# Performance work log

Measured on AMD Instinct MI355X. Metric: run time of the kernel, lower is better.

## Reference

```python
import jax, jax.numpy as jnp
import numpy as np

HID = 2048
NH = 16
HD = HID // NH
FF = 8192
SEQ = 2048
B = 1
EPS = 1e-05
ROPE_BASE = 10000.0


def _layernorm(x, w, b):
    mu = jnp.mean(x, axis=-1, keepdims=True)
    var = jnp.mean(jnp.square(x - mu), axis=-1, keepdims=True)
    return (x - mu) * jax.lax.rsqrt(var + EPS) * w + b


def _rope(x, offset):
    # x: [B, S, H, D]; rotate-half LLaMA-style rotary embedding
    S, D = x.shape[1], x.shape[3]
    inv_freq = 1.0 / (ROPE_BASE ** (jnp.arange(0, D, 2, dtype=jnp.float32) / D))  # [D/2]
    pos = jnp.arange(S, dtype=jnp.float32) + offset
    ang = pos[:, None] * inv_freq[None, :]                     # [S, D/2]
    cos = jnp.cos(ang)[None, :, None, :]                       # [1,S,1,D/2]
    sin = jnp.sin(ang)[None, :, None, :]
    x1, x2 = x[..., : D // 2], x[..., D // 2 :]
    return jnp.concatenate([x1 * cos - x2 * sin, x2 * cos + x1 * sin], axis=-1)


def setup_inputs() -> dict:
    key = jax.random.key(0)
    ks = jax.random.split(key, 16)
    sd = 0.02
    inp = {
        "hidden_states": jax.random.normal(ks[0], (B, SEQ, HID), dtype=jnp.float32),
        # additive causal mask as fed to multi_head_attention_forward
        "attention_mask": jnp.where(
            jnp.tril(jnp.ones((SEQ, SEQ), dtype=bool)), 0.0, -1e9
        ).astype(jnp.float32),
        "ln1_w": jnp.ones((HID,), jnp.float32),
        "ln1_b": jnp.zeros((HID,), jnp.float32),
        "ln2_w": jnp.ones((HID,), jnp.float32),
        "ln2_b": jnp.zeros((HID,), jnp.float32),
        "wq": jax.random.normal(ks[1], (HID, HID), jnp.float32) * sd,
        "bq": jnp.zeros((HID,), jnp.float32),
        "wk": jax.random.normal(ks[2], (HID, HID), jnp.float32) * sd,
        "bk": jnp.zeros((HID,), jnp.float32),
        "wv": jax.random.normal(ks[3], (HID, HID), jnp.float32) * sd,
        "bv": jnp.zeros((HID,), jnp.float32),
        "wo": jax.random.normal(ks[4], (HID, HID), jnp.float32) * sd,
        "bo": jnp.zeros((HID,), jnp.float32),
        "w_gate": jax.random.normal(ks[5], (FF, HID), jnp.float32) * sd,
        "w_up": jax.random.normal(ks[6], (FF, HID), jnp.float32) * sd,
        "w_down": jax.random.normal(ks[7], (HID, FF), jnp.float32) * sd,
        "total_seq_len": SEQ,
    }
    return inp


def reference(hidden_states, attention_mask, ln1_w, ln1_b, ln2_w, ln2_b,
              wq, bq, wk, bk, wv, bv, wo, bo, w_gate, w_up, w_down,
              total_seq_len):
    Bv, S, _ = hidden_states.shape
    x = _layernorm(hidden_states, ln1_w, ln1_b)
    q = (x @ wq.T + bq).reshape(Bv, S, NH, HD)
    k = (x @ wk.T + bk).reshape(Bv, S, NH, HD)
    v = (x @ wv.T + bv).reshape(Bv, S, NH, HD)
    offset = total_seq_len - S  # 0 for prefill
    q = _rope(q, offset)
    k = _rope(k, offset)
    # cache of max_sequence_length zeros concatenated with k/v then sliced to the
    # last total_seq_len entries == just the current k/v when total_seq_len == S
    scale = 1.0 / np.sqrt(HD)
    scores = jnp.einsum("bshd,bthd->bhst", q, k) * scale + attention_mask[None, None]
    probs = jax.nn.softmax(scores, axis=-1)
    attn = jnp.einsum("bhst,bthd->bshd", probs, v).reshape(Bv, S, HID)
    attn = attn @ wo.T + bo
    h = hidden_states + attn
    y = _layernorm(h, ln2_w, ln2_b)
    ffn = (jax.nn.silu(y @ w_gate.T) * (y @ w_up.T)) @ w_down.T
    return h + ffn
```

## Files before the change

kernel.cpp:

```cpp
#include <hip/hip_runtime.h>

#define HIDN 2048
#define NHEAD 16
#define HDIM 128
#define FFDIM 8192
#define SEQLEN 2048

typedef __attribute__((ext_vector_type(8))) __bf16 bf16x8;
typedef __attribute__((ext_vector_type(4))) float f32x4;
typedef __attribute__((ext_vector_type(4))) unsigned short u16x4;
typedef __attribute__((ext_vector_type(8))) unsigned short u16x8;

__device__ __forceinline__ unsigned short f2bfu(float f) {
    unsigned int u = __float_as_uint(f);
    unsigned int r = u + 0x7fffu + ((u >> 16) & 1u);
    return (unsigned short)(r >> 16);
}
__device__ __forceinline__ float bfu2f(unsigned short u) {
    return __uint_as_float(((unsigned int)u) << 16);
}

__device__ __forceinline__ void gload16(const void* g, void* l) {
    __builtin_amdgcn_global_load_lds(
        (const __attribute__((address_space(1))) unsigned int*)g,
        (__attribute__((address_space(3))) unsigned int*)l,
        16, 0, 0);
}

__global__ __launch_bounds__(256)
void conv_f32_bf16(const float* __restrict__ src, unsigned short* __restrict__ dst) {
    int i = blockIdx.x * 256 + threadIdx.x;
    float4 a = ((const float4*)src)[i * 2];
    float4 b = ((const float4*)src)[i * 2 + 1];
    u16x8 v;
    v[0] = f2bfu(a.x); v[1] = f2bfu(a.y); v[2] = f2bfu(a.z); v[3] = f2bfu(a.w);
    v[4] = f2bfu(b.x); v[5] = f2bfu(b.y); v[6] = f2bfu(b.z); v[7] = f2bfu(b.w);
    *(u16x8*)(dst + (size_t)i * 8) = v;
}

__global__ __launch_bounds__(256)
void conv3_f32_bf16(const float* __restrict__ s0, const float* __restrict__ s1,
                    const float* __restrict__ s2, unsigned short* __restrict__ dst) {
    int i = blockIdx.x * 256 + threadIdx.x;
    int m = i >> 19;
    int li = i & ((1 << 19) - 1);
    const float* s = (m == 0) ? s0 : (m == 1) ? s1 : s2;
    float4 a = ((const float4*)s)[li * 2];
    float4 b = ((const float4*)s)[li * 2 + 1];
    u16x8 v;
    v[0] = f2bfu(a.x); v[1] = f2bfu(a.y); v[2] = f2bfu(a.z); v[3] = f2bfu(a.w);
    v[4] = f2bfu(b.x); v[5] = f2bfu(b.y); v[6] = f2bfu(b.z); v[7] = f2bfu(b.w);
    *(u16x8*)(dst + (size_t)i * 8) = v;
}

__global__ __launch_bounds__(256)
void ln_bf16(const float* __restrict__ x, const float* __restrict__ w,
             const float* __restrict__ b, unsigned short* __restrict__ out) {
    const int row = blockIdx.x;
    const int tid = threadIdx.x;
    const float* xr = x + (size_t)row * HIDN;
    float4 v0 = ((const float4*)xr)[tid];
    float4 v1 = ((const float4*)xr)[tid + 256];
    float s = v0.x + v0.y + v0.z + v0.w + v1.x + v1.y + v1.z + v1.w;
    float q = v0.x*v0.x + v0.y*v0.y + v0.z*v0.z + v0.w*v0.w
            + v1.x*v1.x + v1.y*v1.y + v1.z*v1.z + v1.w*v1.w;
    for (int o = 32; o > 0; o >>= 1) {
        s += __shfl_down(s, o, 64);
        q += __shfl_down(q, o, 64);
    }
    __shared__ float red[8];
    const int wid = tid >> 6;
    if ((tid & 63) == 0) { red[wid] = s; red[4 + wid] = q; }
    __syncthreads();
    float st = red[0] + red[1] + red[2] + red[3];
    float qt = red[4] + red[5] + red[6] + red[7];
    float mu = st * (1.0f / HIDN);
    float var = qt * (1.0f / HIDN) - mu * mu;
    float rs = rsqrtf(var + 1e-5f);
    unsigned short* orow = out + (size_t)row * HIDN;
    int i0 = tid * 4, i1 = (tid + 256) * 4;
    orow[i0 + 0] = f2bfu((v0.x - mu) * rs * w[i0 + 0] + b[i0 + 0]);
    orow[i0 + 1] = f2bfu((v0.y - mu) * rs * w[i0 + 1] + b[i0 + 1]);
    orow[i0 + 2] = f2bfu((v0.z - mu) * rs * w[i0 + 2] + b[i0 + 2]);
    orow[i0 + 3] = f2bfu((v0.w - mu) * rs * w[i0 + 3] + b[i0 + 3]);
    orow[i1 + 0] = f2bfu((v1.x - mu) * rs * w[i1 + 0] + b[i1 + 0]);
    orow[i1 + 1] = f2bfu((v1.y - mu) * rs * w[i1 + 1] + b[i1 + 1]);
    orow[i1 + 2] = f2bfu((v1.z - mu) * rs * w[i1 + 2] + b[i1 + 2]);
    orow[i1 + 3] = f2bfu((v1.w - mu) * rs * w[i1 + 3] + b[i1 + 3]);
}

__global__ __launch_bounds__(256)
void wo_ln(const unsigned short* __restrict__ part, const float* __restrict__ h,
           const float* __restrict__ bo, const float* __restrict__ w,
           const float* __restrict__ b, float* __restrict__ out,
           unsigned short* __restrict__ ybf) {
    const int row = blockIdx.x;
    const int tid = threadIdx.x;
    const int c0 = tid * 4, c1 = (tid + 256) * 4;
    float4 o0 = ((const float4*)(h + (size_t)row * HIDN))[tid];
    float4 o1 = ((const float4*)(h + (size_t)row * HIDN))[tid + 256];
    o0.x += bo[c0]; o0.y += bo[c0 + 1]; o0.z += bo[c0 + 2]; o0.w += bo[c0 + 3];
    o1.x += bo[c1]; o1.y += bo[c1 + 1]; o1.z += bo[c1 + 2]; o1.w += bo[c1 + 3];
#pragma unroll
    for (int sk = 0; sk < 4; ++sk) {
        const unsigned short* pr = part + (size_t)sk * 4194304 + (size_t)row * HIDN;
        u16x4 p0 = *(const u16x4*)(pr + c0);
        u16x4 p1 = *(const u16x4*)(pr + c1);
        o0.x += bfu2f(p0[0]); o0.y += bfu2f(p0[1]); o0.z += bfu2f(p0[2]); o0.w += bfu2f(p0[3]);
        o1.x += bfu2f(p1[0]); o1.y += bfu2f(p1[1]); o1.z += bfu2f(p1[2]); o1.w += bfu2f(p1[3]);
    }
    ((float4*)(out + (size_t)row * HIDN))[tid] = o0;
    ((float4*)(out + (size_t)row * HIDN))[tid + 256] = o1;
    float s = o0.x + o0.y + o0.z + o0.w + o1.x + o1.y + o1.z + o1.w;
    float q = o0.x*o0.x + o0.y*o0.y + o0.z*o0.z + o0.w*o0.w
            + o1.x*o1.x + o1.y*o1.y + o1.z*o1.z + o1.w*o1.w;
    for (int o = 32; o > 0; o >>= 1) {
        s += __shfl_down(s, o, 64);
        q += __shfl_down(q, o, 64);
    }
    __shared__ float red[8];
    const int wid = tid >> 6;
    if ((tid & 63) == 0) { red[wid] = s; red[4 + wid] = q; }
    __syncthreads();
    float st = red[0] + red[1] + red[2] + red[3];
    float qt = red[4] + red[5] + red[6] + red[7];
    float mu = st * (1.0f / HIDN);
    float var = qt * (1.0f / HIDN) - mu * mu;
    float rs = rsqrtf(var + 1e-5f);
    unsigned short* yr = ybf + (size_t)row * HIDN;
    yr[c0 + 0] = f2bfu((o0.x - mu) * rs * w[c0 + 0] + b[c0 + 0]);
    yr[c0 + 1] = f2bfu((o0.y - mu) * rs * w[c0 + 1] + b[c0 + 1]);
    yr[c0 + 2] = f2bfu((o0.z - mu) * rs * w[c0 + 2] + b[c0 + 2]);
    yr[c0 + 3] = f2bfu((o0.w - mu) * rs * w[c0 + 3] + b[c0 + 3]);
    yr[c1 + 0] = f2bfu((o1.x - mu) * rs * w[c1 + 0] + b[c1 + 0]);
    yr[c1 + 1] = f2bfu((o1.y - mu) * rs * w[c1 + 1] + b[c1 + 1]);
    yr[c1 + 2] = f2bfu((o1.z - mu) * rs * w[c1 + 2] + b[c1 + 2]);
    yr[c1 + 3] = f2bfu((o1.w - mu) * rs * w[c1 + 3] + b[c1 + 3]);
}

__global__ __launch_bounds__(256)
void rope_kernel(unsigned short* __restrict__ qk, const int* __restrict__ tsl) {
    int id = blockIdx.x * 256 + threadIdx.x;
    int p  = id & 63;
    int hh = (id >> 6) & 31;
    int s  = id >> 11;
    int off = tsl[0] - SEQLEN;
    float inv = exp2f((float)p * -0.20762050593f);
    float ang = (float)(s + off) * inv;
    float c, sn;
    __sincosf(ang, &sn, &c);
    size_t base = (size_t)s * 4096 + hh * 128 + p;
    float x1 = bfu2f(qk[base]);
    float x2 = bfu2f(qk[base + 64]);
    qk[base]      = f2bfu(x1 * c - x2 * sn);
    qk[base + 64] = f2bfu(x2 * c + x1 * sn);
}

#define BAR __builtin_amdgcn_s_barrier()
#define VM4 asm volatile("s_waitcnt vmcnt(4)" ::: "memory")
#define VM0 asm volatile("s_waitcnt vmcnt(0)" ::: "memory")
#define LGK4 do { asm volatile("s_waitcnt lgkmcnt(4)" ::: "memory"); \
                  __builtin_amdgcn_sched_barrier(0); } while (0)
#define LGK0 do { asm volatile("s_waitcnt lgkmcnt(0)" ::: "memory"); \
                  __builtin_amdgcn_sched_barrier(0); } while (0)

#define STAGE_A(tile, h) { const int k0_ = k_start + (tile) * 64;                      \
  _Pragma("unroll") for (int i_ = 0; i_ < 2; ++i_) {                                   \
    int d_ = (h) * 16384 + i_ * 8192 + tid * 16;                                       \
    int r_ = d_ >> 7;                                                                  \
    int cb_ = (d_ & 127) ^ ((r_ & 7) << 4);                                            \
    gload16((const char*)Ab + ((size_t)(brow + r_) * lda + k0_) * 2 + cb_,             \
            smem + ((tile) & 1) * 65536 + (h) * 16384 + i_ * 8192 + w * 1024); } }

#define STAGE_B(tile, h) { const int k0_ = k_start + (tile) * 64;                      \
  _Pragma("unroll") for (int i_ = 0; i_ < 2; ++i_) {                                   \
    int d_ = (h) * 16384 + i_ * 8192 + tid * 16;                                       \
    int r_ = d_ >> 7;                                                                  \
    int cb_ = (d_ & 127) ^ ((r_ & 7) << 4);                                            \
    gload16((const char*)Bb + ((size_t)(bcol + r_) * ldb + k0_) * 2 + cb_,             \
            smem + ((tile) & 1) * 65536 + 32768 + (h) * 16384 + i_ * 8192 + w * 1024); } }

#define LDB(BO)                                                                        \
  _Pragma("unroll") for (int n_ = 0; n_ < 4; ++n_)                                     \
  _Pragma("unroll") for (int kk_ = 0; kk_ < 2; ++kk_)                                  \
    bF[n_][kk_] = *(const bf16x8*)(smem + (BO) + bbase + n_ * 2048 + colb[kk_]);

#define LDA_SET(BO, MP, SET)                                                           \
  _Pragma("unroll") for (int dm_ = 0; dm_ < 2; ++dm_)                                  \
  _Pragma("unroll") for (int kk_ = 0; kk_ < 2; ++kk_)                                  \
    SET[dm_][kk_] = *(const bf16x8*)(smem + (BO) + abase + ((MP) * 2 + dm_) * 2048 + colb[kk_]);

#define MM_SET(SET, MP)                                                                \
  __builtin_amdgcn_s_setprio(1);                                                       \
  _Pragma("unroll") for (int dm_ = 0; dm_ < 2; ++dm_)                                  \
  _Pragma("unroll") for (int n_ = 0; n_ < 4; ++n_)                                     \
  _Pragma("unroll") for (int kk_ = 0; kk_ < 2; ++kk_)                                  \
    acc[(MP) * 2 + dm_][n_] = __builtin_amdgcn_mfma_f32_16x16x32_bf16(                 \
        SET[dm_][kk_], bF[n_][kk_], acc[(MP) * 2 + dm_][n_], 0, 0, 0);                 \
  __builtin_amdgcn_s_setprio(0);

template<int EPI>
__global__ __launch_bounds__(512, 1)
void gemm256(const unsigned short* __restrict__ Ab, int lda,
             const unsigned short* __restrict__ Bb, int ldb,
             int k_len, int nbx, int ldc,
             const float* __restrict__ bias0, const float* __restrict__ bias1,
             const float* __restrict__ bias2,
             unsigned short* __restrict__ outB, unsigned short* __restrict__ outV) {
    extern __shared__ char smem[];
    const int tid = threadIdx.x;
    const int w = tid >> 6, lane = tid & 63;
    const int lr = lane & 15, lg = lane >> 4;
    const int wrow = (w >> 2) * 128;
    const int wc = w & 3;

    const int cpx = nbx >> 3;
    const int xcd = blockIdx.x & 7;
    const int loc = blockIdx.x >> 3;
    const int bx = xcd * cpx + loc % cpx;
    const int by = loc / cpx;
    const int brow = by * 256, bcol = bx * 256;
    const int k_start = blockIdx.y * k_len;

    const int xorv = (lr & 7) << 4;
    int colb[2];
    colb[0] = (lg * 16) ^ xorv;
    colb[1] = (64 + lg * 16) ^ xorv;
    const int abase = (wrow + lr) * 128;
    const int bbase = 32768 + (wc * 64 + lr) * 128;

    f32x4 acc[8][4];
#pragma unroll
    for (int m = 0; m < 8; ++m)
#pragma unroll
        for (int n = 0; n < 4; ++n) acc[m][n] = (f32x4){0.f, 0.f, 0.f, 0.f};

    bf16x8 bF[4][2], aFa[2][2], aFb[2][2];

    const int NT = k_len >> 6;
    const int NIT = NT >> 1;

    STAGE_A(0, 0); STAGE_A(0, 1); STAGE_B(0, 0); STAGE_B(0, 1);
    STAGE_B(1, 0); STAGE_B(1, 1);
    VM4; BAR;
    LDB(0); LDA_SET(0, 0, aFa);

    for (int it = 0; it < NIT; ++it) {
        const int T = 2 * it;
        const bool s2 = (T + 2) < NT, s3 = (T + 3) < NT;
        STAGE_A(T + 1, 0); LDA_SET(0, 1, aFb); LGK4; MM_SET(aFa, 0);
        STAGE_A(T + 1, 1); LDA_SET(0, 2, aFa); LGK4; MM_SET(aFb, 1);
        BAR;
        if (s2) STAGE_B(T + 2, 0);
        LDA_SET(0, 3, aFb); LGK4; MM_SET(aFa, 2);
        if (s2) STAGE_B(T + 2, 1);
        LGK0; MM_SET(aFb, 3);
        if (s2) { VM4; } else { VM0; }
        BAR;
        LDB(65536); LDA_SET(65536, 0, aFa);
        if (s2) STAGE_A(T + 2, 0);
        LDA_SET(65536, 1, aFb); LGK4; MM_SET(aFa, 0);
        if (s2) STAGE_A(T + 2, 1);
        LDA_SET(65536, 2, aFa); LGK4; MM_SET(aFb, 1);
        BAR;
        if (s3) STAGE_B(T + 3, 0);
        LDA_SET(65536, 3, aFb); LGK4; MM_SET(aFa, 2);
        if (s3) STAGE_B(T + 3, 1);
        LGK0; MM_SET(aFb, 3);
        if (s3) { VM4; } else { VM0; }
        BAR;
        LDB(0); LDA_SET(0, 0, aFa);
    }

    char* sw = smem + w * 16384;
    const bool vblk = (EPI == 0) && (bcol >= 4096);

    if (!vblk) {
#pragma unroll
        for (int n = 0; n < 4; ++n) {
            const int col = bcol + wc * 64 + n * 16 + lr;
            float bv = 0.f;
            if (EPI == 0) bv = (col < 2048) ? bias0[col] : bias1[col - 2048];
#pragma unroll
            for (int m = 0; m < 8; ++m)
#pragma unroll
                for (int j = 0; j < 4; ++j) {
                    const int r = m * 16 + lg * 4 + j;
                    const int cb = ((n * 16 + lr) * 2) ^ ((r & 7) << 4);
                    *(unsigned short*)(sw + r * 128 + cb) = f2bfu(acc[m][n][j] + bv);
                }
        }
        const int rl = lane >> 3, cl = lane & 7;
#pragma unroll
        for (int it2 = 0; it2 < 16; ++it2) {
            const int r = it2 * 8 + rl;
            const int cb = (cl * 16) ^ ((r & 7) << 4);
            u16x8 val = *(const u16x8*)(sw + r * 128 + cb);
            const int gr = brow + wrow + r;
            const int gcol = bcol + wc * 64 + cl * 8;
            if (EPI == 0) {
                *(u16x8*)(outB + (size_t)gr * 4096 + gcol) = val;
            } else if (EPI == 1) {
                *(u16x8*)(outB + (size_t)gr * ldc + gcol) = val;
            } else if (EPI == 3) {
                unsigned short* gp = outB + (size_t)gr * ldc + gcol;
                u16x8 gv = *(const u16x8*)gp;
                u16x8 ov;
#pragma unroll
                for (int e = 0; e < 8; ++e) {
                    float g = bfu2f(gv[e]);
                    float uu = bfu2f(val[e]);
                    ov[e] = f2bfu(g / (1.0f + __expf(-g)) * uu);
                }
                *(u16x8*)gp = ov;
            } else {
                *(u16x8*)(outB + (size_t)blockIdx.y * 4194304 + (size_t)gr * ldc + gcol) = val;
            }
        }
    } else {
#pragma unroll
        for (int n = 0; n < 4; ++n) {
            const int c = n * 16 + lr;
            const float bv = bias2[bcol - 4096 + wc * 64 + c];
            const int cx = (c & 7) << 4;
#pragma unroll
            for (int m = 0; m < 8; ++m) {
                const int r0 = m * 16 + lg * 4;
                u16x4 pk;
#pragma unroll
                for (int j = 0; j < 4; ++j) pk[j] = f2bfu(acc[m][n][j] + bv);
                *(u16x4*)(sw + c * 256 + ((r0 * 2) ^ cx)) = pk;
            }
        }
        const int cg = lane >> 4, rl2 = lane & 15;
#pragma unroll
        for (int it2 = 0; it2 < 16; ++it2) {
            const int c = it2 * 4 + cg;
            const int rb = (rl2 * 16) ^ ((c & 7) << 4);
            u16x8 val = *(const u16x8*)(sw + c * 256 + rb);
            const int d = bcol - 4096 + wc * 64 + c;
            *(u16x8*)(outV + (size_t)d * SEQLEN + brow + wrow + rl2 * 8) = val;
        }
    }
}

__global__ __launch_bounds__(256)
void reduce4_add(const unsigned short* __restrict__ part, float* __restrict__ out) {
    int i = blockIdx.x * 256 + threadIdx.x;
    float4 o = ((const float4*)out)[i];
#pragma unroll
    for (int sk = 0; sk < 4; ++sk) {
        u16x4 p = ((const u16x4*)(part + (size_t)sk * 4194304))[i];
        o.x += bfu2f(p[0]); o.y += bfu2f(p[1]); o.z += bfu2f(p[2]); o.w += bfu2f(p[3]);
    }
    ((float4*)out)[i] = o;
}

#define PST 72
__global__ __launch_bounds__(256)
void attn_kernel(const unsigned short* __restrict__ QK, const unsigned short* __restrict__ VT,
                 unsigned short* __restrict__ O) {
    __shared__ __align__(16) unsigned short Ks[2][64 * 128];
    __shared__ __align__(16) unsigned short Vs[2][128 * 64];
    __shared__ __align__(16) unsigned short Ps[4][16 * PST];
    const int tid = threadIdx.x;
    const int lane = tid & 63;
    const int w = tid >> 6;
    const int lr = lane & 15, lg = lane >> 4;

    const int id = blockIdx.x;
    const int h = ((id & 7) << 1) | ((id >> 3) & 1);
    const int p = id >> 4;

    const unsigned short* Kb = QK + 2048 + h * 128;
    const unsigned short* Vb = VT + (size_t)(h * 128) * SEQLEN;

    int krow[4], kcb[4], vrow[4], vcb[4];
#pragma unroll
    for (int ch = 0; ch < 4; ++ch) {
        int d = ch * 4096 + w * 1024 + lane * 16;
        krow[ch] = d >> 8;
        kcb[ch]  = (d & 255) ^ ((krow[ch] & 7) << 4);
        vrow[ch] = d >> 7;
        vcb[ch]  = (d & 127) ^ ((vrow[ch] & 7) << 4);
    }

    const float sc = 0.08838834764831845f;

#pragma unroll 1
    for (int seg = 0; seg < 2; ++seg) {
        const int qb = seg ? (31 - p) : p;
        const int qw = qb * 64 + w * 16;
        const unsigned short* Qb = QK + (size_t)qw * 4096 + h * 128;

        bf16x8 qa[4];
#pragma unroll
        for (int c = 0; c < 4; ++c)
            qa[c] = *(const bf16x8*)(Qb + (size_t)lr * 4096 + c * 32 + lg * 8);

        f32x4 acc[8];
#pragma unroll
        for (int dt = 0; dt < 8; ++dt) acc[dt] = (f32x4){0.f, 0.f, 0.f, 0.f};
        float mrow[4] = {-INFINITY, -INFINITY, -INFINITY, -INFINITY};
        float lrow[4] = {0.f, 0.f, 0.f, 0.f};
        const int ntile = qb + 1;

#pragma unroll
        for (int ch = 0; ch < 4; ++ch) {
            gload16(Kb + (size_t)krow[ch] * 4096 + (kcb[ch] >> 1),
                    (char*)&Ks[0][0] + ch * 4096 + w * 1024);
            gload16(Vb + (size_t)vrow[ch] * SEQLEN + (vcb[ch] >> 1),
                    (char*)&Vs[0][0] + ch * 4096 + w * 1024);
        }
        __syncthreads();

        for (int tt = 0; tt < ntile; ++tt) {
            const int cur = tt & 1;
            const int t0 = tt * 64;
            if (tt + 1 < ntile) {
                const int t1 = t0 + 64;
#pragma unroll
                for (int ch = 0; ch < 4; ++ch) {
                    gload16(Kb + (size_t)(t1 + krow[ch]) * 4096 + (kcb[ch] >> 1),
                            (char*)&Ks[cur ^ 1][0] + ch * 4096 + w * 1024);
                    gload16(Vb + (size_t)vrow[ch] * SEQLEN + t1 + (vcb[ch] >> 1),
                            (char*)&Vs[cur ^ 1][0] + ch * 4096 + w * 1024);
                }
            }
            f32x4 s[4];
#pragma unroll
            for (int th = 0; th < 4; ++th) s[th] = (f32x4){0.f, 0.f, 0.f, 0.f};
            __builtin_amdgcn_s_setprio(1);
#pragma unroll
            for (int th = 0; th < 4; ++th) {
                const int row = th * 16 + lr;
#pragma unroll
                for (int c = 0; c < 4; ++c) {
                    bf16x8 kb = *(const bf16x8*)((char*)&Ks[cur][0] + row * 256 +
                                                 ((c * 64 + lg * 16) ^ ((lr & 7) << 4)));
                    s[th] = __builtin_amdgcn_mfma_f32_16x16x32_bf16(qa[c], kb, s[th], 0, 0, 0);
                }
            }
            __builtin_amdgcn_s_setprio(0);
#pragma unroll
            for (int th = 0; th < 4; ++th) {
                int tg = t0 + th * 16 + lr;
#pragma unroll
                for (int jj = 0; jj < 4; ++jj) {
                    int qg = qw + lg * 4 + jj;
                    s[th][jj] = s[th][jj] * sc + (tg <= qg ? 0.f : -1e9f);
                }
            }
            float mt[4];
#pragma unroll
            for (int jj = 0; jj < 4; ++jj)
                mt[jj] = fmaxf(fmaxf(s[0][jj], s[1][jj]), fmaxf(s[2][jj], s[3][jj]));
#pragma unroll
            for (int o = 8; o > 0; o >>= 1)
#pragma unroll
                for (int jj = 0; jj < 4; ++jj) mt[jj] = fmaxf(mt[jj], __shfl_xor(mt[jj], o, 16));
            bool need = false;
#pragma unroll
            for (int jj = 0; jj < 4; ++jj) need = need || (mt[jj] > mrow[jj] + 4.0f);
            if (__any(need)) {
#pragma unroll
                for (int jj = 0; jj < 4; ++jj) {
                    float mn = fmaxf(mrow[jj], mt[jj]);
                    float a = __expf(mrow[jj] - mn);
                    mrow[jj] = mn;
                    lrow[jj] *= a;
#pragma unroll
                    for (int dt = 0; dt < 8; ++dt) acc[dt][jj] *= a;
                }
            }
            float ps[4] = {0.f, 0.f, 0.f, 0.f};
#pragma unroll
            for (int th = 0; th < 4; ++th)
#pragma unroll
                for (int jj = 0; jj < 4; ++jj) {
                    float pp = __expf(s[th][jj] - mrow[jj]);
                    s[th][jj] = pp;
                    ps[jj] += pp;
                }
#pragma unroll
            for (int o = 8; o > 0; o >>= 1)
#pragma unroll
                for (int jj = 0; jj < 4; ++jj) ps[jj] += __shfl_xor(ps[jj], o, 16);
#pragma unroll
            for (int jj = 0; jj < 4; ++jj) lrow[jj] += ps[jj];
#pragma unroll
            for (int th = 0; th < 4; ++th)
#pragma unroll
                for (int jj = 0; jj < 4; ++jj)
                    Ps[w][(lg * 4 + jj) * PST + th * 16 + lr] = f2bfu(s[th][jj]);
            bf16x8 pa[2];
#pragma unroll
            for (int ks = 0; ks < 2; ++ks)
                pa[ks] = *(const bf16x8*)&Ps[w][lr * PST + ks * 32 + lg * 8];
            __builtin_amdgcn_s_setprio(1);
#pragma unroll
            for (int dt = 0; dt < 8; ++dt) {
                const int d = dt * 16 + lr;
#pragma unroll
                for (int ks = 0; ks < 2; ++ks) {
                    bf16x8 vb = *(const bf16x8*)((char*)&Vs[cur][0] + d * 128 +
                                                 ((ks * 64 + lg * 16) ^ ((lr & 7) << 4)));
                    acc[dt] = __builtin_amdgcn_mfma_f32_16x16x32_bf16(pa[ks], vb, acc[dt], 0, 0, 0);
                }
            }
            __builtin_amdgcn_s_setprio(0);
            __syncthreads();
        }
        float invl[4];
#pragma unroll
        for (int jj = 0; jj < 4; ++jj) invl[jj] = 1.0f / lrow[jj];
#pragma unroll
        for (int dt = 0; dt < 8; ++dt)
#pragma unroll
            for (int jj = 0; jj < 4; ++jj)
                O[(size_t)(qw + lg * 4 + jj) * HIDN + h * HDIM + dt * 16 + lr] =
                    f2bfu(acc[dt][jj] * invl[jj]);
    }
}

extern "C" void kernel_launch(void* const* d_in, const int* in_sizes, int n_in,
                              void* d_out, int out_size, void* d_ws, size_t ws_size,
                              hipStream_t stream) {
    const float* hidden = (const float*)d_in[0];
    const float* ln1w = (const float*)d_in[2];
    const float* ln1b = (const float*)d_in[3];
    const float* ln2w = (const float*)d_in[4];
    const float* ln2b = (const float*)d_in[5];
    const float* wq = (const float*)d_in[6];
    const float* bq = (const float*)d_in[7];
    const float* wk = (const float*)d_in[8];
    const float* bk = (const float*)d_in[9];
    const float* wv = (const float*)d_in[10];
    const float* bv = (const float*)d_in[11];
    const float* wo = (const float*)d_in[12];
    const float* bo = (const float*)d_in[13];
    const float* wg = (const float*)d_in[14];
    const float* wu = (const float*)d_in[15];
    const float* wd = (const float*)d_in[16];
    const int* tsl = (const int*)d_in[17];
    float* out = (float*)d_out;

    char* ws = (char*)d_ws;
    const size_t MB = 1024 * 1024;
    unsigned short* Wbuf = (unsigned short*)(ws);
    unsigned short* qk   = (unsigned short*)(ws + 32 * MB);
    unsigned short* vt   = (unsigned short*)(ws + 48 * MB);
    unsigned short* x_bf = (unsigned short*)(ws + 56 * MB);
    unsigned short* g_bf = (unsigned short*)(ws + 64 * MB);
    unsigned short* part = qk;
    unsigned short* y_bf = vt;

    const int HID2 = HIDN * HIDN;
    const int CONV_HID = HID2 / 8 / 256;
    const int CONV_FF  = FFDIM * HIDN / 8 / 256;
    const size_t LDSZ = 131072;

    conv3_f32_bf16<<<3 * CONV_HID, 256, 0, stream>>>(wq, wk, wv, Wbuf);
    ln_bf16<<<SEQLEN, 256, 0, stream>>>(hidden, ln1w, ln1b, x_bf);
    gemm256<0><<<dim3(192, 1), 512, LDSZ, stream>>>(x_bf, HIDN, Wbuf, HIDN, HIDN, 24, 0,
                                                    bq, bk, bv, qk, vt);
    rope_kernel<<<SEQLEN * 32 * 64 / 256, 256, 0, stream>>>(qk, tsl);
    attn_kernel<<<256, 256, 0, stream>>>(qk, vt, x_bf);

    conv_f32_bf16<<<CONV_HID, 256, 0, stream>>>(wo, Wbuf);
    gemm256<4><<<dim3(64, 4), 512, LDSZ, stream>>>(x_bf, HIDN, Wbuf, HIDN, 512, 8, HIDN,
                                                   nullptr, nullptr, nullptr, g_bf, nullptr);
    wo_ln<<<SEQLEN, 256, 0, stream>>>(g_bf, hidden, bo, ln2w, ln2b, out, y_bf);

    conv_f32_bf16<<<CONV_FF, 256, 0, stream>>>(wg, Wbuf);
    gemm256<1><<<dim3(256, 1), 512, LDSZ, stream>>>(y_bf, HIDN, Wbuf, HIDN, HIDN, 32, FFDIM,
                                                    nullptr, nullptr, nullptr, g_bf, nullptr);
    conv_f32_bf16<<<CONV_FF, 256, 0, stream>>>(wu, Wbuf);
    gemm256<3><<<dim3(256, 1), 512, LDSZ, stream>>>(y_bf, HIDN, Wbuf, HIDN, HIDN, 32, FFDIM,
                                                    nullptr, nullptr, nullptr, g_bf, nullptr);
    conv_f32_bf16<<<CONV_FF, 256, 0, stream>>>(wd, Wbuf);
    gemm256<4><<<dim3(64, 4), 512, LDSZ, stream>>>(g_bf, FFDIM, Wbuf, FFDIM, 2048, 8, HIDN,
                                                   nullptr, nullptr, nullptr, part, nullptr);
    reduce4_add<<<4096, 256, 0, stream>>>(part, out);
}
```

Measured before the change: 442.2 us.

## Fuse fp32-to-bf16 weight conversion into GEMM B-operand loads

Removes the separate weight conversion kernels and has each GEMM load fp32 weights straight into registers, convert them to bf16 and store them to LDS. This drops the extra write and re-read of the converted weight buffers and several launches. In exchange the B path no longer uses direct global-to-LDS loads, the main loop is rescheduled with more barriers and a single A-fragment set, and each block reads twice as many weight bytes from global memory.

```diff
diff --git a/kernel.cpp b/kernel.cpp
--- a/kernel.cpp
+++ b/kernel.cpp
@@ -25,32 +25,6 @@
         (const __attribute__((address_space(1))) unsigned int*)g,
         (__attribute__((address_space(3))) unsigned int*)l,
         16, 0, 0);
-}
-
-__global__ __launch_bounds__(256)
-void conv_f32_bf16(const float* __restrict__ src, unsigned short* __restrict__ dst) {
-    int i = blockIdx.x * 256 + threadIdx.x;
-    float4 a = ((const float4*)src)[i * 2];
-    float4 b = ((const float4*)src)[i * 2 + 1];
-    u16x8 v;
-    v[0] = f2bfu(a.x); v[1] = f2bfu(a.y); v[2] = f2bfu(a.z); v[3] = f2bfu(a.w);
-    v[4] = f2bfu(b.x); v[5] = f2bfu(b.y); v[6] = f2bfu(b.z); v[7] = f2bfu(b.w);
-    *(u16x8*)(dst + (size_t)i * 8) = v;
-}
-
-__global__ __launch_bounds__(256)
-void conv3_f32_bf16(const float* __restrict__ s0, const float* __restrict__ s1,
-                    const float* __restrict__ s2, unsigned short* __restrict__ dst) {
-    int i = blockIdx.x * 256 + threadIdx.x;
-    int m = i >> 19;
-    int li = i & ((1 << 19) - 1);
-    const float* s = (m == 0) ? s0 : (m == 1) ? s1 : s2;
-    float4 a = ((const float4*)s)[li * 2];
-    float4 b = ((const float4*)s)[li * 2 + 1];
-    u16x8 v;
-    v[0] = f2bfu(a.x); v[1] = f2bfu(a.y); v[2] = f2bfu(a.z); v[3] = f2bfu(a.w);
-    v[4] = f2bfu(b.x); v[5] = f2bfu(b.y); v[6] = f2bfu(b.z); v[7] = f2bfu(b.w);
-    *(u16x8*)(dst + (size_t)i * 8) = v;
 }
 
 __global__ __launch_bounds__(256)
@@ -156,13 +130,10 @@
     qk[base + 64] = f2bfu(x2 * c + x1 * sn);
 }
 
-#define BAR __builtin_amdgcn_s_barrier()
+#define BAR asm volatile("s_barrier" ::: "memory")
 #define VM4 asm volatile("s_waitcnt vmcnt(4)" ::: "memory")
 #define VM0 asm volatile("s_waitcnt vmcnt(0)" ::: "memory")
-#define LGK4 do { asm volatile("s_waitcnt lgkmcnt(4)" ::: "memory"); \
-                  __builtin_amdgcn_sched_barrier(0); } while (0)
-#define LGK0 do { asm volatile("s_waitcnt lgkmcnt(0)" ::: "memory"); \
-                  __builtin_amdgcn_sched_barrier(0); } while (0)
+#define LGK0 asm volatile("s_waitcnt lgkmcnt(0)" ::: "memory")
 
 #define STAGE_A(tile, h) { const int k0_ = k_start + (tile) * 64;                      \
   _Pragma("unroll") for (int i_ = 0; i_ < 2; ++i_) {                                   \
@@ -172,37 +143,49 @@
     gload16((const char*)Ab + ((size_t)(brow + r_) * lda + k0_) * 2 + cb_,             \
             smem + ((tile) & 1) * 65536 + (h) * 16384 + i_ * 8192 + w * 1024); } }
 
-#define STAGE_B(tile, h) { const int k0_ = k_start + (tile) * 64;                      \
+#define BLOAD(tile, h) { const int k0_ = k_start + (tile) * 64;                        \
   _Pragma("unroll") for (int i_ = 0; i_ < 2; ++i_) {                                   \
     int d_ = (h) * 16384 + i_ * 8192 + tid * 16;                                       \
     int r_ = d_ >> 7;                                                                  \
     int cb_ = (d_ & 127) ^ ((r_ & 7) << 4);                                            \
-    gload16((const char*)Bb + ((size_t)(bcol + r_) * ldb + k0_) * 2 + cb_,             \
-            smem + ((tile) & 1) * 65536 + 32768 + (h) * 16384 + i_ * 8192 + w * 1024); } }
+    const float* sp_ = Bp + (size_t)(brow_b + r_) * ldb + k0_ + (cb_ >> 1);            \
+    breg[(h)][i_][0] = *(const float4*)sp_;                                            \
+    breg[(h)][i_][1] = *(const float4*)(sp_ + 4); } }
+
+#define BSTORE(tile, h) {                                                              \
+  _Pragma("unroll") for (int i_ = 0; i_ < 2; ++i_) {                                   \
+    int d_ = (h) * 16384 + i_ * 8192 + tid * 16;                                       \
+    float4 lo_ = breg[(h)][i_][0], hi_ = breg[(h)][i_][1];                             \
+    bf16x8 o_;                                                                         \
+    o_[0] = (__bf16)lo_.x; o_[1] = (__bf16)lo_.y; o_[2] = (__bf16)lo_.z;               \
+    o_[3] = (__bf16)lo_.w; o_[4] = (__bf16)hi_.x; o_[5] = (__bf16)hi_.y;               \
+    o_[6] = (__bf16)hi_.z; o_[7] = (__bf16)hi_.w;                                      \
+    *(bf16x8*)(smem + ((tile) & 1) * 65536 + 32768 + d_) = o_; } }
 
 #define LDB(BO)                                                                        \
   _Pragma("unroll") for (int n_ = 0; n_ < 4; ++n_)                                     \
   _Pragma("unroll") for (int kk_ = 0; kk_ < 2; ++kk_)                                  \
     bF[n_][kk_] = *(const bf16x8*)(smem + (BO) + bbase + n_ * 2048 + colb[kk_]);
 
-#define LDA_SET(BO, MP, SET)                                                           \
+#define LDA2(BO, MP)                                                                   \
   _Pragma("unroll") for (int dm_ = 0; dm_ < 2; ++dm_)                                  \
   _Pragma("unroll") for (int kk_ = 0; kk_ < 2; ++kk_)                                  \
-    SET[dm_][kk_] = *(const bf16x8*)(smem + (BO) + abase + ((MP) * 2 + dm_) * 2048 + colb[kk_]);
-
-#define MM_SET(SET, MP)                                                                \
+    aF[dm_][kk_] = *(const bf16x8*)(smem + (BO) + abase + ((MP) * 2 + dm_) * 2048 + colb[kk_]);
+
+#define MM(MP)                                                                         \
   __builtin_amdgcn_s_setprio(1);                                                       \
   _Pragma("unroll") for (int dm_ = 0; dm_ < 2; ++dm_)                                  \
   _Pragma("unroll") for (int n_ = 0; n_ < 4; ++n_)                                     \
   _Pragma("unroll") for (int kk_ = 0; kk_ < 2; ++kk_)                                  \
     acc[(MP) * 2 + dm_][n_] = __builtin_amdgcn_mfma_f32_16x16x32_bf16(                 \
-        SET[dm_][kk_], bF[n_][kk_], acc[(MP) * 2 + dm_][n_], 0, 0, 0);                 \
+        aF[dm_][kk_], bF[n_][kk_], acc[(MP) * 2 + dm_][n_], 0, 0, 0);                  \
   __builtin_amdgcn_s_setprio(0);
 
 template<int EPI>
 __global__ __launch_bounds__(512, 1)
 void gemm256(const unsigned short* __restrict__ Ab, int lda,
-             const unsigned short* __restrict__ Bb, int ldb,
+             const float* __restrict__ B0, const float* __restrict__ B1,
+             const float* __restrict__ B2, int ldb,
              int k_len, int nbx, int ldc,
              const float* __restrict__ bias0, const float* __restrict__ bias1,
              const float* __restrict__ bias2,
@@ -222,6 +205,9 @@
     const int brow = by * 256, bcol = bx * 256;
     const int k_start = blockIdx.y * k_len;
 
+    const float* Bp = (EPI == 0) ? ((bcol < 2048) ? B0 : (bcol < 4096) ? B1 : B2) : B0;
+    const int brow_b = (EPI == 0) ? (bcol & 2047) : bcol;
+
     const int xorv = (lr & 7) << 4;
     int colb[2];
     colb[0] = (lg * 16) ^ xorv;
@@ -235,41 +221,36 @@
 #pragma unroll
         for (int n = 0; n < 4; ++n) acc[m][n] = (f32x4){0.f, 0.f, 0.f, 0.f};
 
-    bf16x8 bF[4][2], aFa[2][2], aFb[2][2];
+    bf16x8 bF[4][2], aF[2][2];
+    float4 breg[2][2][2];
 
     const int NT = k_len >> 6;
     const int NIT = NT >> 1;
 
-    STAGE_A(0, 0); STAGE_A(0, 1); STAGE_B(0, 0); STAGE_B(0, 1);
-    STAGE_B(1, 0); STAGE_B(1, 1);
-    VM4; BAR;
-    LDB(0); LDA_SET(0, 0, aFa);
+    STAGE_A(0, 0); STAGE_A(0, 1);
+    BLOAD(0, 0); BLOAD(0, 1);
+    VM0;
+    BSTORE(0, 0); BSTORE(0, 1);
+    BLOAD(1, 0); BLOAD(1, 1);
+    LGK0; BAR;
 
     for (int it = 0; it < NIT; ++it) {
         const int T = 2 * it;
-        const bool s2 = (T + 2) < NT, s3 = (T + 3) < NT;
-        STAGE_A(T + 1, 0); LDA_SET(0, 1, aFb); LGK4; MM_SET(aFa, 0);
-        STAGE_A(T + 1, 1); LDA_SET(0, 2, aFa); LGK4; MM_SET(aFb, 1);
-        BAR;
-        if (s2) STAGE_B(T + 2, 0);
-        LDA_SET(0, 3, aFb); LGK4; MM_SET(aFa, 2);
-        if (s2) STAGE_B(T + 2, 1);
-        LGK0; MM_SET(aFb, 3);
+        const bool s2 = (T + 2) < NT;
+        LDB(0); LDA2(0, 0); STAGE_A(T + 1, 0); MM(0); BAR;
+        LDA2(0, 1); STAGE_A(T + 1, 1); VM4; BSTORE(T + 1, 0); BSTORE(T + 1, 1); MM(1); BAR;
+        LDA2(0, 2); if (s2) BLOAD(T + 2, 0); MM(2); BAR;
+        LDA2(0, 3); if (s2) BLOAD(T + 2, 1); MM(3);
         if (s2) { VM4; } else { VM0; }
         BAR;
-        LDB(65536); LDA_SET(65536, 0, aFa);
-        if (s2) STAGE_A(T + 2, 0);
-        LDA_SET(65536, 1, aFb); LGK4; MM_SET(aFa, 0);
-        if (s2) STAGE_A(T + 2, 1);
-        LDA_SET(65536, 2, aFa); LGK4; MM_SET(aFb, 1);
+        LDB(65536); LDA2(65536, 0); if (s2) STAGE_A(T + 2, 0); MM(0); BAR;
+        LDA2(65536, 1); if (s2) STAGE_A(T + 2, 1);
+        if (s2) { VM4; BSTORE(T + 2, 0); BSTORE(T + 2, 1); }
+        MM(1); BAR;
+        LDA2(65536, 2); if (s2) BLOAD(T + 3, 0); MM(2); BAR;
+        LDA2(65536, 3); if (s2) BLOAD(T + 3, 1); MM(3);
+        if (s2) { VM4; } else { VM0; }
         BAR;
-        if (s3) STAGE_B(T + 3, 0);
-        LDA_SET(65536, 3, aFb); LGK4; MM_SET(aFa, 2);
-        if (s3) STAGE_B(T + 3, 1);
-        LGK0; MM_SET(aFb, 3);
-        if (s3) { VM4; } else { VM0; }
-        BAR;
-        LDB(0); LDA_SET(0, 0, aFa);
     }
 
     char* sw = smem + w * 16384;
@@ -547,39 +528,34 @@
 
     char* ws = (char*)d_ws;
     const size_t MB = 1024 * 1024;
-    unsigned short* Wbuf = (unsigned short*)(ws);
-    unsigned short* qk   = (unsigned short*)(ws + 32 * MB);
-    unsigned short* vt   = (unsigned short*)(ws + 48 * MB);
-    unsigned short* x_bf = (unsigned short*)(ws + 56 * MB);
-    unsigned short* g_bf = (unsigned short*)(ws + 64 * MB);
+    unsigned short* qk   = (unsigned short*)(ws);
+    unsigned short* vt   = (unsigned short*)(ws + 16 * MB);
+    unsigned short* x_bf = (unsigned short*)(ws + 24 * MB);
+    unsigned short* g_bf = (unsigned short*)(ws + 32 * MB);
     unsigned short* part = qk;
     unsigned short* y_bf = vt;
 
-    const int HID2 = HIDN * HIDN;
-    const int CONV_HID = HID2 / 8 / 256;
-    const int CONV_FF  = FFDIM * HIDN / 8 / 256;
     const size_t LDSZ = 131072;
 
-    conv3_f32_bf16<<<3 * CONV_HID, 256, 0, stream>>>(wq, wk, wv, Wbuf);
     ln_bf16<<<SEQLEN, 256, 0, stream>>>(hidden, ln1w, ln1b, x_bf);
-    gemm256<0><<<dim3(192, 1), 512, LDSZ, stream>>>(x_bf, HIDN, Wbuf, HIDN, HIDN, 24, 0,
-                                                    bq, bk, bv, qk, vt);
+    gemm256<0><<<dim3(192, 1), 512, LDSZ, stream>>>(x_bf, HIDN, wq, wk, wv, HIDN,
+                                                    HIDN, 24, 0, bq, bk, bv, qk, vt);
     rope_kernel<<<SEQLEN * 32 * 64 / 256, 256, 0, stream>>>(qk, tsl);
     attn_kernel<<<256, 256, 0, stream>>>(qk, vt, x_bf);
 
-    conv_f32_bf16<<<CONV_HID, 256, 0, stream>>>(wo, Wbuf);
-    gemm256<4><<<dim3(64, 4), 512, LDSZ, stream>>>(x_bf, HIDN, Wbuf, HIDN, 512, 8, HIDN,
-                                                   nullptr, nullptr, nullptr, g_bf, nullptr);
+    gemm256<4><<<dim3(64, 4), 512, LDSZ, stream>>>(x_bf, HIDN, wo, wo, wo, HIDN,
+                                                   512, 8, HIDN, nullptr, nullptr, nullptr,
+                                                   g_bf, nullptr);
     wo_ln<<<SEQLEN, 256, 0, stream>>>(g_bf, hidden, bo, ln2w, ln2b, out, y_bf);
 
-    conv_f32_bf16<<<CONV_FF, 256, 0, stream>>>(wg, Wbuf);
-    gemm256<1><<<dim3(256, 1), 512, LDSZ, stream>>>(y_bf, HIDN, Wbuf, HIDN, HIDN, 32, FFDIM,
-                                                    nullptr, nullptr, nullptr, g_bf, nullptr);
-    conv_f32_bf16<<<CONV_FF, 256, 0, stream>>>(wu, Wbuf);
-    gemm256<3><<<dim3(256, 1), 512, LDSZ, stream>>>(y_bf, HIDN, Wbuf, HIDN, HIDN, 32, FFDIM,
-                                                    nullptr, nullptr, nullptr, g_bf, nullptr);
-    conv_f32_bf16<<<CONV_FF, 256, 0, stream>>>(wd, Wbuf);
-    gemm256<4><<<dim3(64, 4), 512, LDSZ, stream>>>(g_bf, FFDIM, Wbuf, FFDIM, 2048, 8, HIDN,
-                                                   nullptr, nullptr, nullptr, part, nullptr);
+    gemm256<1><<<dim3(256, 1), 512, LDSZ, stream>>>(y_bf, HIDN, wg, wg, wg, HIDN,
+                                                    HIDN, 32, FFDIM, nullptr, nullptr, nullptr,
+                                                    g_bf, nullptr);
+    gemm256<3><<<dim3(256, 1), 512, LDSZ, stream>>>(y_bf, HIDN, wu, wu, wu, HIDN,
+                                                    HIDN, 32, FFDIM, nullptr, nullptr, nullptr,
+                                                    g_bf, nullptr);
+    gemm256<4><<<dim3(64, 4), 512, LDSZ, stream>>>(g_bf, FFDIM, wd, wd, wd, FFDIM,
+                                                   2048, 8, HIDN, nullptr, nullptr, nullptr,
+                                                   part, nullptr);
     reduce4_add<<<4096, 256, 0, stream>>>(part, out);
 }
```

Measured after the change: 627.2 us. 41.8% more time.

## Replace register double-buffered GEMM main loop with barrier-fenced load-then-compute phases

Applied to the files above, without the earlier changes.

The GEMM main loop drops the double-buffered A-fragment registers (aFa/aFb) that overlapped LDS reads with MFMA. It now loads each fragment set, waits with lgkmcnt(0), and computes, with a workgroup barrier before and after every MFMA group. The barrier macro becomes inline asm and the sched_barrier fences are removed. This lowers register pressure and gives a simpler, ping-pong-style schedule, but exposes LDS latency and adds many extra barriers per k-tile.

```diff
diff --git a/kernel.cpp b/kernel.cpp
--- a/kernel.cpp
+++ b/kernel.cpp
@@ -156,13 +156,10 @@
     qk[base + 64] = f2bfu(x2 * c + x1 * sn);
 }
 
-#define BAR __builtin_amdgcn_s_barrier()
+#define BAR asm volatile("s_barrier" ::: "memory")
 #define VM4 asm volatile("s_waitcnt vmcnt(4)" ::: "memory")
 #define VM0 asm volatile("s_waitcnt vmcnt(0)" ::: "memory")
-#define LGK4 do { asm volatile("s_waitcnt lgkmcnt(4)" ::: "memory"); \
-                  __builtin_amdgcn_sched_barrier(0); } while (0)
-#define LGK0 do { asm volatile("s_waitcnt lgkmcnt(0)" ::: "memory"); \
-                  __builtin_amdgcn_sched_barrier(0); } while (0)
+#define LGK0 asm volatile("s_waitcnt lgkmcnt(0)" ::: "memory")
 
 #define STAGE_A(tile, h) { const int k0_ = k_start + (tile) * 64;                      \
   _Pragma("unroll") for (int i_ = 0; i_ < 2; ++i_) {                                   \
@@ -185,18 +182,18 @@
   _Pragma("unroll") for (int kk_ = 0; kk_ < 2; ++kk_)                                  \
     bF[n_][kk_] = *(const bf16x8*)(smem + (BO) + bbase + n_ * 2048 + colb[kk_]);
 
-#define LDA_SET(BO, MP, SET)                                                           \
+#define LDA2(BO, MP)                                                                   \
   _Pragma("unroll") for (int dm_ = 0; dm_ < 2; ++dm_)                                  \
   _Pragma("unroll") for (int kk_ = 0; kk_ < 2; ++kk_)                                  \
-    SET[dm_][kk_] = *(const bf16x8*)(smem + (BO) + abase + ((MP) * 2 + dm_) * 2048 + colb[kk_]);
-
-#define MM_SET(SET, MP)                                                                \
+    aF[dm_][kk_] = *(const bf16x8*)(smem + (BO) + abase + ((MP) * 2 + dm_) * 2048 + colb[kk_]);
+
+#define MM(MP)                                                                         \
   __builtin_amdgcn_s_setprio(1);                                                       \
   _Pragma("unroll") for (int dm_ = 0; dm_ < 2; ++dm_)                                  \
   _Pragma("unroll") for (int n_ = 0; n_ < 4; ++n_)                                     \
   _Pragma("unroll") for (int kk_ = 0; kk_ < 2; ++kk_)                                  \
     acc[(MP) * 2 + dm_][n_] = __builtin_amdgcn_mfma_f32_16x16x32_bf16(                 \
-        SET[dm_][kk_], bF[n_][kk_], acc[(MP) * 2 + dm_][n_], 0, 0, 0);                 \
+        aF[dm_][kk_], bF[n_][kk_], acc[(MP) * 2 + dm_][n_], 0, 0, 0);                  \
   __builtin_amdgcn_s_setprio(0);
 
 template<int EPI>
@@ -235,7 +232,7 @@
 #pragma unroll
         for (int n = 0; n < 4; ++n) acc[m][n] = (f32x4){0.f, 0.f, 0.f, 0.f};
 
-    bf16x8 bF[4][2], aFa[2][2], aFb[2][2];
+    bf16x8 bF[4][2], aF[2][2];
 
     const int NT = k_len >> 6;
     const int NIT = NT >> 1;
@@ -243,33 +240,22 @@
     STAGE_A(0, 0); STAGE_A(0, 1); STAGE_B(0, 0); STAGE_B(0, 1);
     STAGE_B(1, 0); STAGE_B(1, 1);
     VM4; BAR;
-    LDB(0); LDA_SET(0, 0, aFa);
 
     for (int it = 0; it < NIT; ++it) {
         const int T = 2 * it;
         const bool s2 = (T + 2) < NT, s3 = (T + 3) < NT;
-        STAGE_A(T + 1, 0); LDA_SET(0, 1, aFb); LGK4; MM_SET(aFa, 0);
-        STAGE_A(T + 1, 1); LDA_SET(0, 2, aFa); LGK4; MM_SET(aFb, 1);
-        BAR;
-        if (s2) STAGE_B(T + 2, 0);
-        LDA_SET(0, 3, aFb); LGK4; MM_SET(aFa, 2);
-        if (s2) STAGE_B(T + 2, 1);
-        LGK0; MM_SET(aFb, 3);
+        LDB(0); LDA2(0, 0); STAGE_A(T + 1, 0); BAR; LGK0; MM(0); BAR;
+        LDA2(0, 1); STAGE_A(T + 1, 1); BAR; LGK0; MM(1); BAR;
+        LDA2(0, 2); if (s2) STAGE_B(T + 2, 0); BAR; LGK0; MM(2); BAR;
+        LDA2(0, 3); if (s2) STAGE_B(T + 2, 1);
         if (s2) { VM4; } else { VM0; }
-        BAR;
-        LDB(65536); LDA_SET(65536, 0, aFa);
-        if (s2) STAGE_A(T + 2, 0);
-        LDA_SET(65536, 1, aFb); LGK4; MM_SET(aFa, 0);
-        if (s2) STAGE_A(T + 2, 1);
-        LDA_SET(65536, 2, aFa); LGK4; MM_SET(aFb, 1);
-        BAR;
-        if (s3) STAGE_B(T + 3, 0);
-        LDA_SET(65536, 3, aFb); LGK4; MM_SET(aFa, 2);
-        if (s3) STAGE_B(T + 3, 1);
-        LGK0; MM_SET(aFb, 3);
+        BAR; LGK0; MM(3); BAR;
+        LDB(65536); LDA2(65536, 0); if (s2) STAGE_A(T + 2, 0); BAR; LGK0; MM(0); BAR;
+        LDA2(65536, 1); if (s2) STAGE_A(T + 2, 1); BAR; LGK0; MM(1); BAR;
+        LDA2(65536, 2); if (s3) STAGE_B(T + 3, 0); BAR; LGK0; MM(2); BAR;
+        LDA2(65536, 3); if (s3) STAGE_B(T + 3, 1);
         if (s3) { VM4; } else { VM0; }
-        BAR;
-        LDB(0); LDA_SET(0, 0, aFa);
+        BAR; LGK0; MM(3); BAR;
     }
 
     char* sw = smem + w * 16384;
```

Result: slower. 454.0 us (+2.7%).
